# Kernel tuning notes

Measured on AMD Instinct MI355X. Metric: run time of the kernel, lower is better.

Reference implementation:

```python
import jax, jax.numpy as jnp
import numpy as np

HIDDEN = 1024
FFN = 4 * HIDDEN
E = 8
K = 2
N = 16384


def setup_inputs() -> dict:
    key = jax.random.key(0)
    ks = jax.random.split(key, 7)
    s_in = 1.0 / np.sqrt(HIDDEN)
    s_ffn = 1.0 / np.sqrt(FFN)
    return {
        "x": jax.random.normal(ks[0], (N, HIDDEN), dtype=jnp.float32),
        "Wg": jax.random.uniform(ks[1], (HIDDEN, E), jnp.float32, -s_in, s_in),
        "bg": jax.random.uniform(ks[2], (E,), jnp.float32, -s_in, s_in),
        "W1": jax.random.uniform(ks[3], (E, HIDDEN, FFN), jnp.float32, -s_in, s_in),
        "b1": jax.random.uniform(ks[4], (E, FFN), jnp.float32, -s_in, s_in),
        "W2": jax.random.uniform(ks[5], (E, FFN, HIDDEN), jnp.float32, -s_ffn, s_ffn),
        "b2": jax.random.uniform(ks[6], (E, HIDDEN), jnp.float32, -s_ffn, s_ffn),
    }


def reference(x, Wg, bg, W1, b1, W2, b2):
    # 1. Gating: top-k experts per token, softmax over the k scores
    gate_scores = x @ Wg + bg                              # [N, E]
    topk_scores, topk_idx = jax.lax.top_k(gate_scores, K)  # [N, K]
    topk_w = jax.nn.softmax(topk_scores, axis=-1)          # [N, K]

    # 2+3. Dispatch/compute/combine. Equivalent math: per-token combine weight
    # for expert e is the sum of topk weights of slots routed to e; then
    # out = sum_e cw[:, e] * FFN_e(x). Scan over experts keeps memory bounded.
    n = x.shape[0]
    cw = jnp.zeros((n, E), x.dtype).at[jnp.arange(n)[:, None], topk_idx].add(topk_w)

    def body(acc, packed):
        W1e, b1e, W2e, b2e, cwe = packed
        h = jax.nn.relu(x @ W1e + b1e)      # [N, FFN]
        y = h @ W2e + b2e                   # [N, HIDDEN]
        return acc + cwe[:, None] * y, None

    out, _ = jax.lax.scan(body, jnp.zeros_like(x), (W1, b1, W2, b2, cw.T))
    return out
```

## Files before the change

kernel.cpp:

```cpp
#include <hip/hip_runtime.h>

#define HIDDEN 1024
#define FFN    4096
#define NEXP   8
#define NTOK   16384
#define CAP    16384
#define NPAIRS (2*NTOK)

#define BM 128
#define BN 128
#define BK 32

typedef _Float16 f16;
typedef _Float16 f16x8 __attribute__((ext_vector_type(8)));
typedef float    f32x4 __attribute__((ext_vector_type(4)));

typedef __attribute__((address_space(1))) const unsigned int gu32;
typedef __attribute__((address_space(3))) unsigned int lu32;

__device__ __forceinline__ void gll16(const void* g, void* l) {
  __builtin_amdgcn_global_load_lds((gu32*)g, (lu32*)l, 16, 0, 0);
}


__global__ void k_sentinel(float* out) { if (threadIdx.x == 0) out[0] = -1e30f; }

__global__ void k_zero(float4* out, int n4) {
  int i = blockIdx.x * blockDim.x + threadIdx.x;
  int tot = gridDim.x * blockDim.x;
  for (int j = i; j < n4; j += tot) out[j] = float4{0.f, 0.f, 0.f, 0.f};
}

__global__ void k_cvt(const float* __restrict__ in, f16* __restrict__ out, int n8) {
  int i = blockIdx.x * blockDim.x + threadIdx.x;
  int tot = gridDim.x * blockDim.x;
  for (int j = i; j < n8; j += tot) {
    float4 a = ((const float4*)in)[2 * j];
    float4 b = ((const float4*)in)[2 * j + 1];
    f16x8 v = {(f16)a.x, (f16)a.y, (f16)a.z, (f16)a.w,
               (f16)b.x, (f16)b.y, (f16)b.z, (f16)b.w};
    ((f16x8*)out)[j] = v;
  }
}

__global__ void k_trans(const float* __restrict__ in, f16* __restrict__ out, int R, int C) {
  __shared__ float t[32][33];
  int z = blockIdx.z;
  const float* I = in + (size_t)z * R * C;
  f16* O = out + (size_t)z * R * C;
  int c0 = blockIdx.x * 32, r0 = blockIdx.y * 32;
  int tx = threadIdx.x & 31, ty = threadIdx.x >> 5;
  #pragma unroll
  for (int i = 0; i < 32; i += 8)
    t[ty + i][tx] = I[(size_t)(r0 + ty + i) * C + c0 + tx];
  __syncthreads();
  #pragma unroll
  for (int i = 0; i < 32; i += 8)
    O[(size_t)(c0 + ty + i) * R + r0 + tx] = (f16)t[tx][ty + i];
}

__global__ void k_gate(const float* __restrict__ x, const float* __restrict__ Wg,
                       const float* __restrict__ bg, int2* __restrict__ toke,
                       float2* __restrict__ tokw) {
  int wid = threadIdx.x >> 6, lane = threadIdx.x & 63;
  int tok = blockIdx.x * 4 + wid;
  const float* xr = x + (size_t)tok * HIDDEN;
  float s[8] = {0.f, 0.f, 0.f, 0.f, 0.f, 0.f, 0.f, 0.f};
  for (int j = lane; j < HIDDEN; j += 64) {
    float xv = xr[j];
    const float4* wr = (const float4*)(Wg + j * 8);
    float4 wa = wr[0], wb = wr[1];
    s[0] += xv * wa.x; s[1] += xv * wa.y; s[2] += xv * wa.z; s[3] += xv * wa.w;
    s[4] += xv * wb.x; s[5] += xv * wb.y; s[6] += xv * wb.z; s[7] += xv * wb.w;
  }
  #pragma unroll
  for (int off = 32; off > 0; off >>= 1) {
    #pragma unroll
    for (int e = 0; e < 8; ++e) s[e] += __shfl_down(s[e], off);
  }
  if (lane == 0) {
    float best = -1e30f, second = -1e30f;
    int bi = 0, si = 0;
    #pragma unroll
    for (int e = 0; e < 8; ++e) {
      float v = s[e] + bg[e];
      if (v > best)        { second = best; si = bi; best = v; bi = e; }
      else if (v > second) { second = v; si = e; }
    }
    float p = expf(second - best);
    float inv = 1.0f / (1.0f + p);
    toke[tok] = make_int2(bi, si);
    tokw[tok] = make_float2(inv, p * inv);
  }
}

__global__ void k_build(const int2* __restrict__ toke, const float2* __restrict__ tokw,
                        int* __restrict__ pair_tok, float* __restrict__ pair_w,
                        int* __restrict__ counts) {
  int e = blockIdx.x;
  __shared__ int cursor;
  if (threadIdx.x == 0) cursor = 0;
  __syncthreads();
  for (int i = threadIdx.x; i < NTOK; i += blockDim.x) {
    int2 ee = toke[i];
    float2 ww = tokw[i];
    if (ee.x == e) { int p = atomicAdd(&cursor, 1); pair_tok[e * CAP + p] = i; pair_w[e * CAP + p] = ww.x; }
    if (ee.y == e) { int p = atomicAdd(&cursor, 1); pair_tok[e * CAP + p] = i; pair_w[e * CAP + p] = ww.y; }
  }
  __syncthreads();
  if (threadIdx.x == 0) counts[e] = cursor;
}

__global__ __launch_bounds__(256, 2) void k_ffn1(
    const f16* __restrict__ xh, const f16* __restrict__ w1t,
    const float* __restrict__ b1, f16* __restrict__ hbuf,
    const int* __restrict__ pair_tok, const int* __restrict__ counts) {
  const int e = blockIdx.z;
  const int cnt = counts[e];
  const int m0 = blockIdx.y * BM;
  if (m0 >= cnt) return;
  const int n0 = blockIdx.x * BN;
  int hbase = 0;
  #pragma unroll
  for (int j = 0; j < NEXP; ++j) hbase += (j < e) ? counts[j] : 0;

  __shared__ f16 As[BM][BK];
  __shared__ f16 Bs[BN][BK];
  const int tid = threadIdx.x;
  const int lane = tid & 63, wid = tid >> 6;
  const int wm = (wid & 1) * 64, wn = (wid >> 1) * 64;

  const int sr = lane >> 2, kc = lane & 3;
  const int maxr = cnt - 1 - m0;
  const int* toks = pair_tok + e * CAP + m0;
  const int ra0 = wid * 32 + sr, ra1 = ra0 + 16;
  const f16* aptr0 = xh + (size_t)toks[min(ra0, maxr)] * HIDDEN + kc * 8;
  const f16* aptr1 = xh + (size_t)toks[min(ra1, maxr)] * HIDDEN + kc * 8;
  const f16* bbase = w1t + (size_t)e * FFN * HIDDEN;
  const f16* bptr0 = bbase + (size_t)(n0 + ra0) * HIDDEN + kc * 8;
  const f16* bptr1 = bbase + (size_t)(n0 + ra1) * HIDDEN + kc * 8;

  f32x4 zero4 = {0.f, 0.f, 0.f, 0.f};
  f32x4 acc[4][4];
  #pragma unroll
  for (int m = 0; m < 4; ++m)
    #pragma unroll
    for (int n = 0; n < 4; ++n) acc[m][n] = zero4;

  const int cl = lane & 15, rg = lane >> 4;
  for (int k0 = 0; k0 < HIDDEN; k0 += BK) {
    gll16(aptr0 + k0, &As[wid * 32][0]);
    gll16(aptr1 + k0, &As[wid * 32 + 16][0]);
    gll16(bptr0 + k0, &Bs[wid * 32][0]);
    gll16(bptr1 + k0, &Bs[wid * 32 + 16][0]);
    __syncthreads();
    f16x8 af[4], bf[4];
    #pragma unroll
    for (int m = 0; m < 4; ++m) af[m] = *(const f16x8*)&As[wm + m * 16 + cl][rg * 8];
    #pragma unroll
    for (int n = 0; n < 4; ++n) bf[n] = *(const f16x8*)&Bs[wn + n * 16 + cl][rg * 8];
    #pragma unroll
    for (int m = 0; m < 4; ++m)
      #pragma unroll
      for (int n = 0; n < 4; ++n)
        acc[m][n] = __builtin_amdgcn_mfma_f32_16x16x32_f16(af[m], bf[n], acc[m][n], 0, 0, 0);
    __syncthreads();
  }

  float bias[4];
  #pragma unroll
  for (int n = 0; n < 4; ++n) bias[n] = b1[(size_t)e * FFN + n0 + wn + n * 16 + cl];
  #pragma unroll
  for (int m = 0; m < 4; ++m) {
    #pragma unroll
    for (int i = 0; i < 4; ++i) {
      int rl = wm + m * 16 + rg * 4 + i;
      if (m0 + rl < cnt) {
        f16* hp = hbuf + (size_t)(hbase + m0 + rl) * FFN + n0 + wn + cl;
        #pragma unroll
        for (int n = 0; n < 4; ++n) {
          float v = acc[m][n][i] + bias[n];
          hp[n * 16] = (f16)fmaxf(v, 0.0f);
        }
      }
    }
  }
}

__global__ __launch_bounds__(256, 2) void k_ffn2(
    const f16* __restrict__ hbuf, const f16* __restrict__ w2t,
    const float* __restrict__ b2, float* __restrict__ out,
    const int* __restrict__ pair_tok, const float* __restrict__ pair_w,
    const int* __restrict__ counts) {
  const int e = blockIdx.z;
  const int cnt = counts[e];
  const int m0 = blockIdx.y * BM;
  if (m0 >= cnt) return;
  const int n0 = blockIdx.x * BN;
  int hbase = 0;
  #pragma unroll
  for (int j = 0; j < NEXP; ++j) hbase += (j < e) ? counts[j] : 0;

  __shared__ f16 As[BM][BK];
  __shared__ f16 Bs[BN][BK];
  const int tid = threadIdx.x;
  const int lane = tid & 63, wid = tid >> 6;
  const int wm = (wid & 1) * 64, wn = (wid >> 1) * 64;

  const int sr = lane >> 2, kc = lane & 3;
  const int maxr = cnt - 1 - m0;
  const int ra0 = wid * 32 + sr, ra1 = ra0 + 16;
  const f16* aptr0 = hbuf + (size_t)(hbase + m0 + min(ra0, maxr)) * FFN + kc * 8;
  const f16* aptr1 = hbuf + (size_t)(hbase + m0 + min(ra1, maxr)) * FFN + kc * 8;
  const f16* bbase = w2t + (size_t)e * HIDDEN * FFN;
  const f16* bptr0 = bbase + (size_t)(n0 + ra0) * FFN + kc * 8;
  const f16* bptr1 = bbase + (size_t)(n0 + ra1) * FFN + kc * 8;

  f32x4 zero4 = {0.f, 0.f, 0.f, 0.f};
  f32x4 acc[4][4];
  #pragma unroll
  for (int m = 0; m < 4; ++m)
    #pragma unroll
    for (int n = 0; n < 4; ++n) acc[m][n] = zero4;

  const int cl = lane & 15, rg = lane >> 4;
  for (int k0 = 0; k0 < FFN; k0 += BK) {
    gll16(aptr0 + k0, &As[wid * 32][0]);
    gll16(aptr1 + k0, &As[wid * 32 + 16][0]);
    gll16(bptr0 + k0, &Bs[wid * 32][0]);
    gll16(bptr1 + k0, &Bs[wid * 32 + 16][0]);
    __syncthreads();
    f16x8 af[4], bf[4];
    #pragma unroll
    for (int m = 0; m < 4; ++m) af[m] = *(const f16x8*)&As[wm + m * 16 + cl][rg * 8];
    #pragma unroll
    for (int n = 0; n < 4; ++n) bf[n] = *(const f16x8*)&Bs[wn + n * 16 + cl][rg * 8];
    #pragma unroll
    for (int m = 0; m < 4; ++m)
      #pragma unroll
      for (int n = 0; n < 4; ++n)
        acc[m][n] = __builtin_amdgcn_mfma_f32_16x16x32_f16(af[m], bf[n], acc[m][n], 0, 0, 0);
    __syncthreads();
  }

  float bias[4];
  #pragma unroll
  for (int n = 0; n < 4; ++n) bias[n] = b2[(size_t)e * HIDDEN + n0 + wn + n * 16 + cl];
  #pragma unroll
  for (int m = 0; m < 4; ++m) {
    #pragma unroll
    for (int i = 0; i < 4; ++i) {
      int rl = wm + m * 16 + rg * 4 + i;
      if (m0 + rl < cnt) {
        int p = e * CAP + m0 + rl;
        int tok = pair_tok[p];
        float w = pair_w[p];
        float* op = out + (size_t)tok * HIDDEN + n0 + wn + cl;
        #pragma unroll
        for (int n = 0; n < 4; ++n)
          atomicAdd(&op[n * 16], (acc[m][n][i] + bias[n]) * w);
      }
    }
  }
}


static constexpr size_t alignup(size_t v) { return (v + 255) & ~size_t(255); }

extern "C" void kernel_launch(void* const* d_in, const int* in_sizes, int n_in,
                              void* d_out, int out_size, void* d_ws, size_t ws_size,
                              hipStream_t stream) {
  const float* x  = (const float*)d_in[0];
  const float* Wg = (const float*)d_in[1];
  const float* bg = (const float*)d_in[2];
  const float* W1 = (const float*)d_in[3];
  const float* b1 = (const float*)d_in[4];
  const float* W2 = (const float*)d_in[5];
  const float* b2 = (const float*)d_in[6];
  float* out = (float*)d_out;

  size_t off = 0;
  char* ws = (char*)d_ws;
  auto take = [&](size_t bytes) { void* p = ws + off; off += alignup(bytes); return p; };
  f16*    xh       = (f16*)take((size_t)NTOK * HIDDEN * 2);
  f16*    w1t      = (f16*)take((size_t)NEXP * FFN * HIDDEN * 2);
  f16*    w2t      = (f16*)take((size_t)NEXP * HIDDEN * FFN * 2);
  f16*    hbuf     = (f16*)take((size_t)NPAIRS * FFN * 2);
  int*    pair_tok = (int*)take((size_t)NEXP * CAP * 4);
  float*  pair_w   = (float*)take((size_t)NEXP * CAP * 4);
  int2*   toke     = (int2*)take((size_t)NTOK * 8);
  float2* tokw     = (float2*)take((size_t)NTOK * 8);
  int*    counts   = (int*)take(64);

  if (off > ws_size) {
    k_sentinel<<<1, 64, 0, stream>>>(out);
    return;
  }

  k_zero<<<2048, 256, 0, stream>>>((float4*)out, NTOK * HIDDEN / 4);
  k_cvt<<<2048, 256, 0, stream>>>(x, xh, NTOK * HIDDEN / 8);
  k_trans<<<dim3(FFN / 32, HIDDEN / 32, NEXP), 256, 0, stream>>>(W1, w1t, HIDDEN, FFN);
  k_trans<<<dim3(HIDDEN / 32, FFN / 32, NEXP), 256, 0, stream>>>(W2, w2t, FFN, HIDDEN);
  k_gate<<<NTOK / 4, 256, 0, stream>>>(x, Wg, bg, toke, tokw);
  k_build<<<NEXP, 256, 0, stream>>>(toke, tokw, pair_tok, pair_w, counts);
  k_ffn1<<<dim3(FFN / BN, CAP / BM, NEXP), 256, 0, stream>>>(xh, w1t, b1, hbuf, pair_tok, counts);
  k_ffn2<<<dim3(HIDDEN / BN, CAP / BM, NEXP), 256, 0, stream>>>(hbuf, w2t, b2, out, pair_tok, pair_w, counts);
}
```

Before: 1.259 ms.

## Rewrite expert GEMMs with 256x256x64 double-buffered swizzled LDS pipeline

```diff
diff --git a/kernel.cpp b/kernel.cpp
--- a/kernel.cpp
+++ b/kernel.cpp
@@ -7,9 +7,9 @@
 #define CAP    16384
 #define NPAIRS (2*NTOK)
 
-#define BM 128
-#define BN 128
-#define BK 32
+#define BM 256
+#define BN 256
+#define BK 64
 
 typedef _Float16 f16;
 typedef _Float16 f16x8 __attribute__((ext_vector_type(8)));
@@ -111,154 +111,225 @@
   if (threadIdx.x == 0) counts[e] = cursor;
 }
 
-__global__ __launch_bounds__(256, 2) void k_ffn1(
+__device__ __forceinline__ void gemm_core(
+    const f16* const (&aS)[4], const f16* const (&bS)[4],
+    f16* lsA0, f16* lsA1, f16* lsB0, f16* lsB1,
+    int nt, int sbase, int ra0, int rb0, int sx0, int sx1,
+    f32x4 (&acc)[8][4]) {
+  #pragma unroll
+  for (int c = 0; c < 4; ++c) {
+    gll16(aS[c], lsA0 + sbase + c * 512);
+    gll16(bS[c], lsB0 + sbase + c * 512);
+  }
+  #pragma unroll
+  for (int c = 0; c < 4; ++c) {
+    gll16(aS[c] + 64, lsA1 + sbase + c * 512);
+    gll16(bS[c] + 64, lsB1 + sbase + c * 512);
+  }
+  for (int t = 0; t < nt; ++t) {
+    const f16* LA = (t & 1) ? lsA1 : lsA0;
+    const f16* LB = (t & 1) ? lsB1 : lsB0;
+    if (t + 1 < nt) asm volatile("s_waitcnt vmcnt(8)" ::: "memory");
+    else            asm volatile("s_waitcnt vmcnt(0)" ::: "memory");
+    __builtin_amdgcn_sched_barrier(0);
+    __builtin_amdgcn_s_barrier();
+    __builtin_amdgcn_sched_barrier(0);
+
+    f16x8 af[4][2], bf[4][2];
+    #pragma unroll
+    for (int nf = 0; nf < 4; ++nf) {
+      bf[nf][0] = *(const f16x8*)(LB + rb0 + nf * 1024 + sx0);
+      bf[nf][1] = *(const f16x8*)(LB + rb0 + nf * 1024 + sx1);
+    }
+    #pragma unroll
+    for (int m = 0; m < 4; ++m) {
+      af[m][0] = *(const f16x8*)(LA + ra0 + m * 1024 + sx0);
+      af[m][1] = *(const f16x8*)(LA + ra0 + m * 1024 + sx1);
+    }
+    __builtin_amdgcn_s_setprio(1);
+    #pragma unroll
+    for (int m = 0; m < 4; ++m)
+      #pragma unroll
+      for (int nf = 0; nf < 4; ++nf)
+        acc[m][nf] = __builtin_amdgcn_mfma_f32_16x16x32_f16(af[m][0], bf[nf][0], acc[m][nf], 0, 0, 0);
+    __builtin_amdgcn_s_setprio(0);
+    __builtin_amdgcn_s_setprio(1);
+    #pragma unroll
+    for (int m = 0; m < 4; ++m)
+      #pragma unroll
+      for (int nf = 0; nf < 4; ++nf)
+        acc[m][nf] = __builtin_amdgcn_mfma_f32_16x16x32_f16(af[m][1], bf[nf][1], acc[m][nf], 0, 0, 0);
+    __builtin_amdgcn_s_setprio(0);
+
+    #pragma unroll
+    for (int m = 0; m < 4; ++m) {
+      af[m][0] = *(const f16x8*)(LA + ra0 + (m + 4) * 1024 + sx0);
+      af[m][1] = *(const f16x8*)(LA + ra0 + (m + 4) * 1024 + sx1);
+    }
+    asm volatile("s_waitcnt lgkmcnt(0)" ::: "memory");
+    __builtin_amdgcn_sched_barrier(0);
+    __builtin_amdgcn_s_barrier();
+    __builtin_amdgcn_sched_barrier(0);
+    if (t + 2 < nt) {
+      f16* SA = (t & 1) ? lsA1 : lsA0;
+      f16* SB = (t & 1) ? lsB1 : lsB0;
+      #pragma unroll
+      for (int c = 0; c < 4; ++c) {
+        gll16(aS[c] + (size_t)(t + 2) * 64, SA + sbase + c * 512);
+        gll16(bS[c] + (size_t)(t + 2) * 64, SB + sbase + c * 512);
+      }
+    }
+    __builtin_amdgcn_s_setprio(1);
+    #pragma unroll
+    for (int m = 0; m < 4; ++m)
+      #pragma unroll
+      for (int nf = 0; nf < 4; ++nf)
+        acc[m + 4][nf] = __builtin_amdgcn_mfma_f32_16x16x32_f16(af[m][0], bf[nf][0], acc[m + 4][nf], 0, 0, 0);
+    __builtin_amdgcn_s_setprio(0);
+    __builtin_amdgcn_s_setprio(1);
+    #pragma unroll
+    for (int m = 0; m < 4; ++m)
+      #pragma unroll
+      for (int nf = 0; nf < 4; ++nf)
+        acc[m + 4][nf] = __builtin_amdgcn_mfma_f32_16x16x32_f16(af[m][1], bf[nf][1], acc[m + 4][nf], 0, 0, 0);
+    __builtin_amdgcn_s_setprio(0);
+  }
+}
+
+__global__ __launch_bounds__(512, 2) void k_ffn1(
     const f16* __restrict__ xh, const f16* __restrict__ w1t,
     const float* __restrict__ b1, f16* __restrict__ hbuf,
     const int* __restrict__ pair_tok, const int* __restrict__ counts) {
   const int e = blockIdx.z;
   const int cnt = counts[e];
-  const int m0 = blockIdx.y * BM;
+  const int bid = blockIdx.x;
+  const int x = bid & 7, j = bid >> 3;
+  const int m0 = (j & 63) * BM;
+  const int n0 = (x + 8 * (j >> 6)) * BN;
   if (m0 >= cnt) return;
-  const int n0 = blockIdx.x * BN;
   int hbase = 0;
   #pragma unroll
-  for (int j = 0; j < NEXP; ++j) hbase += (j < e) ? counts[j] : 0;
-
-  __shared__ f16 As[BM][BK];
-  __shared__ f16 Bs[BN][BK];
+  for (int q = 0; q < NEXP; ++q) hbase += (q < e) ? counts[q] : 0;
+
+  __shared__ f16 lsA_[2][BM * BK];
+  __shared__ f16 lsB_[2][BN * BK];
+
   const int tid = threadIdx.x;
   const int lane = tid & 63, wid = tid >> 6;
-  const int wm = (wid & 1) * 64, wn = (wid >> 1) * 64;
-
-  const int sr = lane >> 2, kc = lane & 3;
+  const int wr = wid >> 2, wc = wid & 3;
+  const int cl = lane & 15, rg = lane >> 4;
+  const int sl = lane >> 3, so = lane & 7;
+  const int xslot = (so ^ sl) * 8;
+  const int sbase = wid * 2048;
+  const int ra0 = (wr * 128 + cl) * 64;
+  const int rb0 = (wc * 64 + cl) * 64;
+  const int sx0 = (rg ^ (cl & 7)) * 8;
+  const int sx1 = sx0 ^ 32;
+
   const int maxr = cnt - 1 - m0;
   const int* toks = pair_tok + e * CAP + m0;
-  const int ra0 = wid * 32 + sr, ra1 = ra0 + 16;
-  const f16* aptr0 = xh + (size_t)toks[min(ra0, maxr)] * HIDDEN + kc * 8;
-  const f16* aptr1 = xh + (size_t)toks[min(ra1, maxr)] * HIDDEN + kc * 8;
   const f16* bbase = w1t + (size_t)e * FFN * HIDDEN;
-  const f16* bptr0 = bbase + (size_t)(n0 + ra0) * HIDDEN + kc * 8;
-  const f16* bptr1 = bbase + (size_t)(n0 + ra1) * HIDDEN + kc * 8;
-
-  f32x4 zero4 = {0.f, 0.f, 0.f, 0.f};
-  f32x4 acc[4][4];
-  #pragma unroll
-  for (int m = 0; m < 4; ++m)
-    #pragma unroll
-    for (int n = 0; n < 4; ++n) acc[m][n] = zero4;
-
-  const int cl = lane & 15, rg = lane >> 4;
-  for (int k0 = 0; k0 < HIDDEN; k0 += BK) {
-    gll16(aptr0 + k0, &As[wid * 32][0]);
-    gll16(aptr1 + k0, &As[wid * 32 + 16][0]);
-    gll16(bptr0 + k0, &Bs[wid * 32][0]);
-    gll16(bptr1 + k0, &Bs[wid * 32 + 16][0]);
-    __syncthreads();
-    f16x8 af[4], bf[4];
-    #pragma unroll
-    for (int m = 0; m < 4; ++m) af[m] = *(const f16x8*)&As[wm + m * 16 + cl][rg * 8];
-    #pragma unroll
-    for (int n = 0; n < 4; ++n) bf[n] = *(const f16x8*)&Bs[wn + n * 16 + cl][rg * 8];
-    #pragma unroll
-    for (int m = 0; m < 4; ++m)
-      #pragma unroll
-      for (int n = 0; n < 4; ++n)
-        acc[m][n] = __builtin_amdgcn_mfma_f32_16x16x32_f16(af[m], bf[n], acc[m][n], 0, 0, 0);
-    __syncthreads();
-  }
+  const f16* aS[4]; const f16* bS[4];
+  #pragma unroll
+  for (int c = 0; c < 4; ++c) {
+    int r = wid * 32 + c * 8 + sl;
+    aS[c] = xh + (size_t)toks[min(r, maxr)] * HIDDEN + xslot;
+    bS[c] = bbase + (size_t)(n0 + r) * HIDDEN + xslot;
+  }
+
+  f32x4 acc[8][4];
+  #pragma unroll
+  for (int m = 0; m < 8; ++m)
+    #pragma unroll
+    for (int nf = 0; nf < 4; ++nf) acc[m][nf] = (f32x4){0.f, 0.f, 0.f, 0.f};
+
+  gemm_core(aS, bS, lsA_[0], lsA_[1], lsB_[0], lsB_[1],
+            HIDDEN / BK, sbase, ra0, rb0, sx0, sx1, acc);
 
   float bias[4];
   #pragma unroll
-  for (int n = 0; n < 4; ++n) bias[n] = b1[(size_t)e * FFN + n0 + wn + n * 16 + cl];
-  #pragma unroll
-  for (int m = 0; m < 4; ++m) {
+  for (int nf = 0; nf < 4; ++nf) bias[nf] = b1[(size_t)e * FFN + n0 + wc * 64 + nf * 16 + cl];
+  #pragma unroll
+  for (int m = 0; m < 8; ++m) {
     #pragma unroll
     for (int i = 0; i < 4; ++i) {
-      int rl = wm + m * 16 + rg * 4 + i;
+      int rl = wr * 128 + m * 16 + rg * 4 + i;
       if (m0 + rl < cnt) {
-        f16* hp = hbuf + (size_t)(hbase + m0 + rl) * FFN + n0 + wn + cl;
+        f16* hp = hbuf + (size_t)(hbase + m0 + rl) * FFN + n0 + wc * 64 + cl;
         #pragma unroll
-        for (int n = 0; n < 4; ++n) {
-          float v = acc[m][n][i] + bias[n];
-          hp[n * 16] = (f16)fmaxf(v, 0.0f);
-        }
+        for (int nf = 0; nf < 4; ++nf)
+          hp[nf * 16] = (f16)fmaxf(acc[m][nf][i] + bias[nf], 0.0f);
       }
     }
   }
 }
 
-__global__ __launch_bounds__(256, 2) void k_ffn2(
+__global__ __launch_bounds__(512, 2) void k_ffn2(
     const f16* __restrict__ hbuf, const f16* __restrict__ w2t,
     const float* __restrict__ b2, float* __restrict__ out,
     const int* __restrict__ pair_tok, const float* __restrict__ pair_w,
     const int* __restrict__ counts) {
   const int e = blockIdx.z;
   const int cnt = counts[e];
-  const int m0 = blockIdx.y * BM;
+  const int bid = blockIdx.x;
+  const int x = bid & 7, j = bid >> 3;
+  const int n0 = (j & 3) * BN;
+  const int m0 = (x + 8 * (j >> 2)) * BM;
   if (m0 >= cnt) return;
-  const int n0 = blockIdx.x * BN;
   int hbase = 0;
   #pragma unroll
-  for (int j = 0; j < NEXP; ++j) hbase += (j < e) ? counts[j] : 0;
-
-  __shared__ f16 As[BM][BK];
-  __shared__ f16 Bs[BN][BK];
+  for (int q = 0; q < NEXP; ++q) hbase += (q < e) ? counts[q] : 0;
+
+  __shared__ f16 lsA_[2][BM * BK];
+  __shared__ f16 lsB_[2][BN * BK];
+
   const int tid = threadIdx.x;
   const int lane = tid & 63, wid = tid >> 6;
-  const int wm = (wid & 1) * 64, wn = (wid >> 1) * 64;
-
-  const int sr = lane >> 2, kc = lane & 3;
+  const int wr = wid >> 2, wc = wid & 3;
+  const int cl = lane & 15, rg = lane >> 4;
+  const int sl = lane >> 3, so = lane & 7;
+  const int xslot = (so ^ sl) * 8;
+  const int sbase = wid * 2048;
+  const int ra0 = (wr * 128 + cl) * 64;
+  const int rb0 = (wc * 64 + cl) * 64;
+  const int sx0 = (rg ^ (cl & 7)) * 8;
+  const int sx1 = sx0 ^ 32;
+
   const int maxr = cnt - 1 - m0;
-  const int ra0 = wid * 32 + sr, ra1 = ra0 + 16;
-  const f16* aptr0 = hbuf + (size_t)(hbase + m0 + min(ra0, maxr)) * FFN + kc * 8;
-  const f16* aptr1 = hbuf + (size_t)(hbase + m0 + min(ra1, maxr)) * FFN + kc * 8;
   const f16* bbase = w2t + (size_t)e * HIDDEN * FFN;
-  const f16* bptr0 = bbase + (size_t)(n0 + ra0) * FFN + kc * 8;
-  const f16* bptr1 = bbase + (size_t)(n0 + ra1) * FFN + kc * 8;
-
-  f32x4 zero4 = {0.f, 0.f, 0.f, 0.f};
-  f32x4 acc[4][4];
-  #pragma unroll
-  for (int m = 0; m < 4; ++m)
-    #pragma unroll
-    for (int n = 0; n < 4; ++n) acc[m][n] = zero4;
-
-  const int cl = lane & 15, rg = lane >> 4;
-  for (int k0 = 0; k0 < FFN; k0 += BK) {
-    gll16(aptr0 + k0, &As[wid * 32][0]);
-    gll16(aptr1 + k0, &As[wid * 32 + 16][0]);
-    gll16(bptr0 + k0, &Bs[wid * 32][0]);
-    gll16(bptr1 + k0, &Bs[wid * 32 + 16][0]);
-    __syncthreads();
-    f16x8 af[4], bf[4];
-    #pragma unroll
-    for (int m = 0; m < 4; ++m) af[m] = *(const f16x8*)&As[wm + m * 16 + cl][rg * 8];
-    #pragma unroll
-    for (int n = 0; n < 4; ++n) bf[n] = *(const f16x8*)&Bs[wn + n * 16 + cl][rg * 8];
-    #pragma unroll
-    for (int m = 0; m < 4; ++m)
-      #pragma unroll
-      for (int n = 0; n < 4; ++n)
-        acc[m][n] = __builtin_amdgcn_mfma_f32_16x16x32_f16(af[m], bf[n], acc[m][n], 0, 0, 0);
-    __syncthreads();
-  }
+  const f16* aS[4]; const f16* bS[4];
+  #pragma unroll
+  for (int c = 0; c < 4; ++c) {
+    int r = wid * 32 + c * 8 + sl;
+    aS[c] = hbuf + (size_t)(hbase + m0 + min(r, maxr)) * FFN + xslot;
+    bS[c] = bbase + (size_t)(n0 + r) * FFN + xslot;
+  }
+
+  f32x4 acc[8][4];
+  #pragma unroll
+  for (int m = 0; m < 8; ++m)
+    #pragma unroll
+    for (int nf = 0; nf < 4; ++nf) acc[m][nf] = (f32x4){0.f, 0.f, 0.f, 0.f};
+
+  gemm_core(aS, bS, lsA_[0], lsA_[1], lsB_[0], lsB_[1],
+            FFN / BK, sbase, ra0, rb0, sx0, sx1, acc);
 
   float bias[4];
   #pragma unroll
-  for (int n = 0; n < 4; ++n) bias[n] = b2[(size_t)e * HIDDEN + n0 + wn + n * 16 + cl];
-  #pragma unroll
-  for (int m = 0; m < 4; ++m) {
+  for (int nf = 0; nf < 4; ++nf) bias[nf] = b2[(size_t)e * HIDDEN + n0 + wc * 64 + nf * 16 + cl];
+  #pragma unroll
+  for (int m = 0; m < 8; ++m) {
     #pragma unroll
     for (int i = 0; i < 4; ++i) {
-      int rl = wm + m * 16 + rg * 4 + i;
+      int rl = wr * 128 + m * 16 + rg * 4 + i;
       if (m0 + rl < cnt) {
         int p = e * CAP + m0 + rl;
         int tok = pair_tok[p];
         float w = pair_w[p];
-        float* op = out + (size_t)tok * HIDDEN + n0 + wn + cl;
+        float* op = out + (size_t)tok * HIDDEN + n0 + wc * 64 + cl;
         #pragma unroll
-        for (int n = 0; n < 4; ++n)
-          atomicAdd(&op[n * 16], (acc[m][n][i] + bias[n]) * w);
+        for (int nf = 0; nf < 4; ++nf)
+          atomicAdd(&op[nf * 16], (acc[m][nf][i] + bias[nf]) * w);
       }
     }
   }
@@ -303,6 +374,6 @@
   k_trans<<<dim3(HIDDEN / 32, FFN / 32, NEXP), 256, 0, stream>>>(W2, w2t, FFN, HIDDEN);
   k_gate<<<NTOK / 4, 256, 0, stream>>>(x, Wg, bg, toke, tokw);
   k_build<<<NEXP, 256, 0, stream>>>(toke, tokw, pair_tok, pair_w, counts);
-  k_ffn1<<<dim3(FFN / BN, CAP / BM, NEXP), 256, 0, stream>>>(xh, w1t, b1, hbuf, pair_tok, counts);
-  k_ffn2<<<dim3(HIDDEN / BN, CAP / BM, NEXP), 256, 0, stream>>>(hbuf, w2t, b2, out, pair_tok, pair_w, counts);
-}
+  k_ffn1<<<dim3((FFN / BN) * (CAP / BM), 1, NEXP), 512, 0, stream>>>(xh, w1t, b1, hbuf, pair_tok, counts);
+  k_ffn2<<<dim3((HIDDEN / BN) * (CAP / BM), 1, NEXP), 512, 0, stream>>>(hbuf, w2t, b2, out, pair_tok, pair_w, counts);
+}
```

Measured after the change: 1.270 ms. Within noise of the previous version (+0.9%).
